# Performance work log

Hardware: AMD Instinct MI355X
Metric: run time of the kernel (lower is better)

Reference implementation:

```python
import jax, jax.numpy as jnp
import numpy as np

DIM = 1024

def setup_inputs() -> dict:
    key = jax.random.key(0)
    ks = jax.random.split(key, 8)
    B, Sx, Sy, D = 4, 2048, 2048, DIM
    s = 1.0 / np.sqrt(D)
    return {
        "x": jax.random.normal(ks[0], (B, Sx, D), jnp.float32),
        "y": jax.random.normal(ks[1], (B, Sy, D), jnp.float32),
        "Wq": jax.random.normal(ks[2], (D, D), jnp.float32) * s,
        "bq": jnp.zeros((D,), jnp.float32),
        "Wk": jax.random.normal(ks[3], (D, D), jnp.float32) * s,
        "bk": jnp.zeros((D,), jnp.float32),
        "Wv": jax.random.normal(ks[4], (D, D), jnp.float32) * s,
        "bv": jnp.zeros((D,), jnp.float32),
    }

def reference(x, y, Wq, bq, Wk, bk, Wv, bv):
    D = x.shape[-1]
    scale = jnp.sqrt(jnp.asarray(D, x.dtype))
    Q = jnp.einsum('bsd,de->bse', x, Wq) + bq  # [B,Sx,D]
    K = jnp.einsum('btd,de->bte', y, Wk) + bk  # [B,Sy,D]
    V = jnp.einsum('btd,de->bte', y, Wv) + bv  # [B,Sy,D]
    scores = jnp.einsum('bse,bte->bst', Q, K) / scale  # [B,Sx,Sy]
    probs = jax.nn.softmax(scores, axis=-1)
    out = jnp.einsum('bst,bte->bse', probs, V)  # [B,Sx,D]
    return out
```

## Files before the change

### kernel.cpp

```cpp
#include <hip/hip_runtime.h>

typedef __bf16 bf16x8_t __attribute__((ext_vector_type(8)));
typedef float f32x4_t __attribute__((ext_vector_type(4)));
typedef unsigned short ushort_t;

__device__ __forceinline__ unsigned short f2bf(float f) {
  unsigned u = __float_as_uint(f);
  u = (u + 0x7FFFu + ((u >> 16) & 1u)) >> 16;
  return (unsigned short)u;
}
__device__ __forceinline__ float bf2f(unsigned short h) {
  return __uint_as_float(((unsigned)h) << 16);
}

__device__ __forceinline__ void gload16(const void* g, void* l) {
  __builtin_amdgcn_global_load_lds(
      (const __attribute__((address_space(1))) unsigned int*)g,
      (__attribute__((address_space(3))) unsigned int*)l, 16, 0, 0);
}

#define BARRIER() __builtin_amdgcn_s_barrier()
#define LGKM0()                                        \
  do {                                                 \
    asm volatile("s_waitcnt lgkmcnt(0)" ::: "memory"); \
    __builtin_amdgcn_sched_barrier(0);                 \
  } while (0)

template<bool OUT_BF16, bool HAS_BIAS>
__global__ __launch_bounds__(512, 2)
void gemm256(const ushort_t* __restrict__ A, const ushort_t* __restrict__ Bt,
             void* __restrict__ Cp, const float* __restrict__ bias,
             int gx, int gy, int K, int lda, int ldb, int ldc,
             long sA, long sB, long sC, float alpha)
{
  __shared__ __align__(16) ushort_t sm[2 * 32768];
  const int tid = threadIdx.x;
  const int lane = tid & 63;
  const int w = tid >> 6;
  const int wr = w >> 2, wc = w & 3;

  const int per = gridDim.x >> 3;
  int wg = blockIdx.x;
  wg = (wg & 7) * per + (wg >> 3);
  const int bz = wg / (gx * gy);
  const int rr = wg - bz * gx * gy;
  const int by = rr / gx, bx = rr - by * gx;
  const int bm = by * 256, bn = bx * 256;

  const int srr = lane >> 3;
  const int csw = ((lane & 7) ^ srr) << 3;
  const ushort_t* pA = A + (long)bz * sA + (long)(bm + w * 16 + srr) * lda + csw;
  const ushort_t* pB = Bt + (long)bz * sB + (long)(bn + w * 16 + srr) * ldb + csw;

  auto stA = [&](int buf, int h, int t) {
    const ushort_t* g = pA + (long)(h * 128) * lda + t * 64;
    ushort_t* d = sm + buf * 32768 + h * 8192 + w * 1024;
    gload16(g, d);
    gload16(g + 8 * lda, d + 512);
  };
  auto stB = [&](int buf, int h, int t) {
    const ushort_t* g = pB + (long)(h * 128) * ldb + t * 64;
    ushort_t* d = sm + buf * 32768 + 16384 + h * 8192 + w * 1024;
    gload16(g, d);
    gload16(g + 8 * ldb, d + 512);
  };

  const int q = lane >> 4, x7 = lane & 7;
  const int cx0 = ((0 + q) ^ x7) << 3;
  const int cx1 = ((4 + q) ^ x7) << 3;
  const int abase = wr * 8192 + (lane & 15) * 64;
  const int bbase = 16384 + wc * 4096 + (lane & 15) * 64;

  f32x4_t acc[8][4];
  const f32x4_t z4 = {0.f, 0.f, 0.f, 0.f};
#pragma unroll
  for (int m = 0; m < 8; ++m)
#pragma unroll
    for (int n = 0; n < 4; ++n) acc[m][n] = z4;

  bf16x8_t a[8], blo[4], bhi[4];

  stA(0, 0, 0); stA(0, 1, 0); stB(0, 0, 0); stB(0, 1, 0);
  stB(1, 0, 1); stB(1, 1, 1); stA(1, 0, 1);
  asm volatile("s_waitcnt vmcnt(6)" ::: "memory");
  __builtin_amdgcn_sched_barrier(0);
  BARRIER();

#define LDX(off) __builtin_bit_cast(bf16x8_t, *(const uint4*)(s + (off)))

  const int nt = K >> 6;
  for (int t = 0; t < nt; ++t) {
    const int buf = t & 1;
    const ushort_t* s = sm + buf * 32768;

#pragma unroll
    for (int mf = 0; mf < 4; ++mf) {
      a[mf * 2]     = LDX(abase + mf * 1024 + cx0);
      a[mf * 2 + 1] = LDX(abase + mf * 1024 + cx1);
    }
#pragma unroll
    for (int nf = 0; nf < 2; ++nf) {
      blo[nf * 2]     = LDX(bbase + nf * 1024 + cx0);
      blo[nf * 2 + 1] = LDX(bbase + nf * 1024 + cx1);
    }
    if (t + 1 < nt) stA(buf ^ 1, 1, t + 1);
    BARRIER();
    LGKM0();
    __builtin_amdgcn_s_setprio(1);
#pragma unroll
    for (int mf = 0; mf < 4; ++mf)
#pragma unroll
      for (int nf = 0; nf < 2; ++nf) {
        acc[mf][nf] = __builtin_amdgcn_mfma_f32_16x16x32_bf16(a[mf * 2], blo[nf * 2], acc[mf][nf], 0, 0, 0);
        acc[mf][nf] = __builtin_amdgcn_mfma_f32_16x16x32_bf16(a[mf * 2 + 1], blo[nf * 2 + 1], acc[mf][nf], 0, 0, 0);
      }
    __builtin_amdgcn_s_setprio(0);
    BARRIER();

#pragma unroll
    for (int nf = 0; nf < 2; ++nf) {
      bhi[nf * 2]     = LDX(bbase + (nf + 2) * 1024 + cx0);
      bhi[nf * 2 + 1] = LDX(bbase + (nf + 2) * 1024 + cx1);
    }
    if (t + 2 < nt) stB(buf, 0, t + 2);
    BARRIER();
    LGKM0();
    __builtin_amdgcn_s_setprio(1);
#pragma unroll
    for (int mf = 0; mf < 4; ++mf)
#pragma unroll
      for (int nf = 0; nf < 2; ++nf) {
        acc[mf][nf + 2] = __builtin_amdgcn_mfma_f32_16x16x32_bf16(a[mf * 2], bhi[nf * 2], acc[mf][nf + 2], 0, 0, 0);
        acc[mf][nf + 2] = __builtin_amdgcn_mfma_f32_16x16x32_bf16(a[mf * 2 + 1], bhi[nf * 2 + 1], acc[mf][nf + 2], 0, 0, 0);
      }
    __builtin_amdgcn_s_setprio(0);
    BARRIER();

#pragma unroll
    for (int mf = 0; mf < 4; ++mf) {
      a[mf * 2]     = LDX(abase + (mf + 4) * 1024 + cx0);
      a[mf * 2 + 1] = LDX(abase + (mf + 4) * 1024 + cx1);
    }
    if (t + 2 < nt) stB(buf, 1, t + 2);
    BARRIER();
    LGKM0();
    __builtin_amdgcn_s_setprio(1);
#pragma unroll
    for (int mf = 0; mf < 4; ++mf)
#pragma unroll
      for (int nf = 0; nf < 2; ++nf) {
        acc[mf + 4][nf + 2] = __builtin_amdgcn_mfma_f32_16x16x32_bf16(a[mf * 2], bhi[nf * 2], acc[mf + 4][nf + 2], 0, 0, 0);
        acc[mf + 4][nf + 2] = __builtin_amdgcn_mfma_f32_16x16x32_bf16(a[mf * 2 + 1], bhi[nf * 2 + 1], acc[mf + 4][nf + 2], 0, 0, 0);
      }
    __builtin_amdgcn_s_setprio(0);
    BARRIER();

    if (t + 2 < nt) stA(buf, 0, t + 2);
    __builtin_amdgcn_s_setprio(1);
#pragma unroll
    for (int mf = 0; mf < 4; ++mf)
#pragma unroll
      for (int nf = 0; nf < 2; ++nf) {
        acc[mf + 4][nf] = __builtin_amdgcn_mfma_f32_16x16x32_bf16(a[mf * 2], blo[nf * 2], acc[mf + 4][nf], 0, 0, 0);
        acc[mf + 4][nf] = __builtin_amdgcn_mfma_f32_16x16x32_bf16(a[mf * 2 + 1], blo[nf * 2 + 1], acc[mf + 4][nf], 0, 0, 0);
      }
    __builtin_amdgcn_s_setprio(0);
    if (t + 1 < nt) {
      if (t + 2 < nt) asm volatile("s_waitcnt vmcnt(6)" ::: "memory");
      else            asm volatile("s_waitcnt vmcnt(0)" ::: "memory");
      __builtin_amdgcn_sched_barrier(0);
    }
    BARRIER();
  }
#undef LDX

  const long zC = (long)bz * sC;
  const int r0 = q * 4;
  const int c0 = lane & 15;
#pragma unroll
  for (int mf = 0; mf < 8; ++mf) {
    const int grow0 = bm + wr * 128 + mf * 16 + r0;
#pragma unroll
    for (int nf = 0; nf < 4; ++nf) {
      const int gcol = bn + wc * 64 + nf * 16 + c0;
      float bv_ = 0.f;
      if constexpr (HAS_BIAS) bv_ = bias[gcol];
#pragma unroll
      for (int i = 0; i < 4; ++i) {
        const float v = acc[mf][nf][i] * alpha + bv_;
        if constexpr (OUT_BF16) {
          ((ushort_t*)Cp)[zC + (long)(grow0 + i) * ldc + gcol] = f2bf(v);
        } else {
          ((float*)Cp)[zC + (long)(grow0 + i) * ldc + gcol] = v;
        }
      }
    }
  }
}

template<bool OUT_BF16, bool HAS_BIAS>
__global__ __launch_bounds__(512, 2)
void gemm_hs(const ushort_t* __restrict__ A, const ushort_t* __restrict__ Bt,
             void* __restrict__ Cp, const float* __restrict__ bias,
             int gx, int gy, int K, int lda, int ldb, int ldc,
             long sA, long sB, long sC, float alpha)
{
  __shared__ __align__(16) ushort_t sm[2 * 24576];
  const int tid = threadIdx.x;
  const int lane = tid & 63;
  const int w = tid >> 6;
  const int wr = w >> 2, wc = w & 3;

  const int per = gridDim.x >> 3;
  int wg = blockIdx.x;
  wg = (wg & 7) * per + (wg >> 3);
  const int bz = wg / (gx * gy);
  const int rr = wg - bz * gx * gy;
  const int by = rr / gx, bx = rr - by * gx;
  const int bm = by * 128, bn = bx * 256;

  const int srr = lane >> 3;
  const int csw = ((lane & 7) ^ srr) << 3;
  const ushort_t* pA = A + (long)bz * sA + (long)(bm + w * 16 + srr) * lda + csw;
  const ushort_t* pB = Bt + (long)bz * sB + (long)(bn + w * 32 + srr) * ldb + csw;

  auto stA = [&](int buf, int t) {
    const ushort_t* g = pA + t * 64;
    ushort_t* d = sm + buf * 24576 + w * 1024;
    gload16(g, d);
    gload16(g + 8 * lda, d + 512);
  };
  auto stB = [&](int buf, int t) {
    const ushort_t* g = pB + t * 64;
    ushort_t* d = sm + buf * 24576 + 8192 + w * 2048;
    gload16(g, d);
    gload16(g + 8 * ldb, d + 512);
    gload16(g + 16 * ldb, d + 1024);
    gload16(g + 24 * ldb, d + 1536);
  };

  const int q = lane >> 4, x7 = lane & 7;
  const int cx0 = ((0 + q) ^ x7) << 3;
  const int cx1 = ((4 + q) ^ x7) << 3;
  const int abase = wr * 4096 + (lane & 15) * 64;
  const int bbase = 8192 + wc * 4096 + (lane & 15) * 64;

  f32x4_t acc[4][4];
  const f32x4_t z4 = {0.f, 0.f, 0.f, 0.f};
#pragma unroll
  for (int m = 0; m < 4; ++m)
#pragma unroll
    for (int n = 0; n < 4; ++n) acc[m][n] = z4;

  bf16x8_t a01[4], a23[4], blo[4], bhi[4];

  stA(0, 0); stB(0, 0); stA(1, 1);
  asm volatile("s_waitcnt vmcnt(2)" ::: "memory");
  __builtin_amdgcn_sched_barrier(0);
  BARRIER();

#define LDX(off) __builtin_bit_cast(bf16x8_t, *(const uint4*)(s + (off)))

  const int nt = K >> 6;
  for (int t = 0; t < nt; ++t) {
    const int buf = t & 1;
    const ushort_t* s = sm + buf * 24576;

    a01[0] = LDX(abase + cx0);        a01[1] = LDX(abase + cx1);
    a01[2] = LDX(abase + 1024 + cx0); a01[3] = LDX(abase + 1024 + cx1);
    blo[0] = LDX(bbase + cx0);        blo[1] = LDX(bbase + cx1);
    blo[2] = LDX(bbase + 1024 + cx0); blo[3] = LDX(bbase + 1024 + cx1);
    if (t + 1 < nt) stB(buf ^ 1, t + 1);
    BARRIER();
    LGKM0();
    __builtin_amdgcn_s_setprio(1);
#pragma unroll
    for (int mf = 0; mf < 2; ++mf)
#pragma unroll
      for (int nf = 0; nf < 2; ++nf) {
        acc[mf][nf] = __builtin_amdgcn_mfma_f32_16x16x32_bf16(a01[mf * 2], blo[nf * 2], acc[mf][nf], 0, 0, 0);
        acc[mf][nf] = __builtin_amdgcn_mfma_f32_16x16x32_bf16(a01[mf * 2 + 1], blo[nf * 2 + 1], acc[mf][nf], 0, 0, 0);
      }
    __builtin_amdgcn_s_setprio(0);
    BARRIER();

    bhi[0] = LDX(bbase + 2048 + cx0); bhi[1] = LDX(bbase + 2048 + cx1);
    bhi[2] = LDX(bbase + 3072 + cx0); bhi[3] = LDX(bbase + 3072 + cx1);
    BARRIER();
    LGKM0();
    __builtin_amdgcn_s_setprio(1);
#pragma unroll
    for (int mf = 0; mf < 2; ++mf)
#pragma unroll
      for (int nf = 0; nf < 2; ++nf) {
        acc[mf][nf + 2] = __builtin_amdgcn_mfma_f32_16x16x32_bf16(a01[mf * 2], bhi[nf * 2], acc[mf][nf + 2], 0, 0, 0);
        acc[mf][nf + 2] = __builtin_amdgcn_mfma_f32_16x16x32_bf16(a01[mf * 2 + 1], bhi[nf * 2 + 1], acc[mf][nf + 2], 0, 0, 0);
      }
    __builtin_amdgcn_s_setprio(0);
    BARRIER();

    a23[0] = LDX(abase + 2048 + cx0); a23[1] = LDX(abase + 2048 + cx1);
    a23[2] = LDX(abase + 3072 + cx0); a23[3] = LDX(abase + 3072 + cx1);
    BARRIER();
    LGKM0();
    __builtin_amdgcn_s_setprio(1);
#pragma unroll
    for (int mf = 0; mf < 2; ++mf)
#pragma unroll
      for (int nf = 0; nf < 2; ++nf) {
        acc[mf + 2][nf + 2] = __builtin_amdgcn_mfma_f32_16x16x32_bf16(a23[mf * 2], bhi[nf * 2], acc[mf + 2][nf + 2], 0, 0, 0);
        acc[mf + 2][nf + 2] = __builtin_amdgcn_mfma_f32_16x16x32_bf16(a23[mf * 2 + 1], bhi[nf * 2 + 1], acc[mf + 2][nf + 2], 0, 0, 0);
      }
    __builtin_amdgcn_s_setprio(0);
    BARRIER();

    if (t + 2 < nt) stA(buf, t + 2);
    __builtin_amdgcn_s_setprio(1);
#pragma unroll
    for (int mf = 0; mf < 2; ++mf)
#pragma unroll
      for (int nf = 0; nf < 2; ++nf) {
        acc[mf + 2][nf] = __builtin_amdgcn_mfma_f32_16x16x32_bf16(a23[mf * 2], blo[nf * 2], acc[mf + 2][nf], 0, 0, 0);
        acc[mf + 2][nf] = __builtin_amdgcn_mfma_f32_16x16x32_bf16(a23[mf * 2 + 1], blo[nf * 2 + 1], acc[mf + 2][nf], 0, 0, 0);
      }
    __builtin_amdgcn_s_setprio(0);
    if (t + 1 < nt) {
      if (t + 2 < nt) asm volatile("s_waitcnt vmcnt(2)" ::: "memory");
      else            asm volatile("s_waitcnt vmcnt(0)" ::: "memory");
      __builtin_amdgcn_sched_barrier(0);
    }
    BARRIER();
  }
#undef LDX

  const long zC = (long)bz * sC;
  const int r0 = q * 4;
  const int c0 = lane & 15;
#pragma unroll
  for (int mf = 0; mf < 4; ++mf) {
    const int grow0 = bm + wr * 64 + mf * 16 + r0;
#pragma unroll
    for (int nf = 0; nf < 4; ++nf) {
      const int gcol = bn + wc * 64 + nf * 16 + c0;
      float bv_ = 0.f;
      if constexpr (HAS_BIAS) bv_ = bias[gcol];
#pragma unroll
      for (int i = 0; i < 4; ++i) {
        const float v = acc[mf][nf][i] * alpha + bv_;
        if constexpr (OUT_BF16) {
          ((ushort_t*)Cp)[zC + (long)(grow0 + i) * ldc + gcol] = f2bf(v);
        } else {
          ((float*)Cp)[zC + (long)(grow0 + i) * ldc + gcol] = v;
        }
      }
    }
  }
}

__global__ __launch_bounds__(256)
void conv2(const float* __restrict__ x, const float* __restrict__ y,
           ushort_t* __restrict__ xb, ushort_t* __restrict__ yb) {
  const int b = blockIdx.x;
  const float* in = (b < 4096) ? x : y;
  ushort_t* out = (b < 4096) ? xb : yb;
  const long i = (long)(b & 4095) * 256 + threadIdx.x;
  const float4 a = ((const float4*)in)[i * 2];
  const float4 c = ((const float4*)in)[i * 2 + 1];
  uint4 o;
  o.x = (unsigned)f2bf(a.x) | ((unsigned)f2bf(a.y) << 16);
  o.y = (unsigned)f2bf(a.z) | ((unsigned)f2bf(a.w) << 16);
  o.z = (unsigned)f2bf(c.x) | ((unsigned)f2bf(c.y) << 16);
  o.w = (unsigned)f2bf(c.z) | ((unsigned)f2bf(c.w) << 16);
  ((uint4*)out)[i] = o;
}

__global__ __launch_bounds__(256)
void wtrans3(const float* __restrict__ W0, const float* __restrict__ W1,
             const float* __restrict__ W2, ushort_t* __restrict__ T0,
             ushort_t* __restrict__ T1, ushort_t* __restrict__ T2) {
  const float* W = (blockIdx.z == 0) ? W0 : (blockIdx.z == 1) ? W1 : W2;
  ushort_t* Wt = (blockIdx.z == 0) ? T0 : (blockIdx.z == 1) ? T1 : T2;
  __shared__ float tile[32][33];
  const int bx = blockIdx.x * 32;
  const int by = blockIdx.y * 32;
  const int t = threadIdx.x;
  const int c = t & 31, r0 = t >> 5;
#pragma unroll
  for (int i = 0; i < 4; ++i)
    tile[r0 + i * 8][c] = W[(long)(by + r0 + i * 8) * 1024 + bx + c];
  __syncthreads();
#pragma unroll
  for (int i = 0; i < 4; ++i)
    Wt[(long)(bx + r0 + i * 8) * 1024 + by + c] = f2bf(tile[c][r0 + i * 8]);
}

__global__ __launch_bounds__(256)
void bconcat(const float* __restrict__ a, const float* __restrict__ b,
             float* __restrict__ o) {
  const int i = blockIdx.x * 256 + threadIdx.x;
  o[i] = (i < 1024) ? a[i] : b[i - 1024];
}

__global__ __launch_bounds__(256)
void transpose_bf16(const ushort_t* __restrict__ in, ushort_t* __restrict__ out,
                    int ld_in, int ld_out, long in_bs, long out_bs) {
  __shared__ ushort_t tt[64][65];
  in += (long)blockIdx.z * in_bs;
  out += (long)blockIdx.z * out_bs;
  const int r0 = blockIdx.y * 64, c0 = blockIdx.x * 64;
  const int tc = threadIdx.x & 31;
  const int tr = threadIdx.x >> 5;
#pragma unroll
  for (int i = 0; i < 8; ++i) {
    const unsigned v = *(const unsigned*)(in + (long)(r0 + tr + 8 * i) * ld_in + c0 + tc * 2);
    tt[tr + 8 * i][tc * 2] = (ushort_t)(v & 0xffff);
    tt[tr + 8 * i][tc * 2 + 1] = (ushort_t)(v >> 16);
  }
  __syncthreads();
#pragma unroll
  for (int i = 0; i < 8; ++i) {
    const unsigned v = (unsigned)tt[tc * 2][tr + 8 * i] |
                       ((unsigned)tt[tc * 2 + 1][tr + 8 * i] << 16);
    *(unsigned*)(out + (long)(c0 + tr + 8 * i) * ld_out + r0 + tc * 2) = v;
  }
}

__global__ __launch_bounds__(256)
void softmax_rows(ushort_t* __restrict__ S) {
  const long row = blockIdx.x;
  ushort_t* p = S + row * 2048;
  const int t = threadIdx.x;
  uint4 v = ((uint4*)p)[t];
  ushort_t* hp = (ushort_t*)&v;
  float f[8];
#pragma unroll
  for (int j = 0; j < 8; ++j) f[j] = bf2f(hp[j]);

  float m = f[0];
#pragma unroll
  for (int j = 1; j < 8; ++j) m = fmaxf(m, f[j]);
#pragma unroll
  for (int s = 32; s; s >>= 1) m = fmaxf(m, __shfl_xor(m, s, 64));
  __shared__ float redm[4];
  __shared__ float reds[4];
  const int wave = t >> 6, lane = t & 63;
  if (lane == 0) redm[wave] = m;
  __syncthreads();
  m = fmaxf(fmaxf(redm[0], redm[1]), fmaxf(redm[2], redm[3]));

  float sum = 0.f;
#pragma unroll
  for (int j = 0; j < 8; ++j) { f[j] = __expf(f[j] - m); sum += f[j]; }
#pragma unroll
  for (int s = 32; s; s >>= 1) sum += __shfl_xor(sum, s, 64);
  if (lane == 0) reds[wave] = sum;
  __syncthreads();
  sum = reds[0] + reds[1] + reds[2] + reds[3];
  const float inv = 1.0f / sum;
#pragma unroll
  for (int j = 0; j < 8; ++j) hp[j] = f2bf(f[j] * inv);
  ((uint4*)p)[t] = v;
}

extern "C" void kernel_launch(void* const* d_in, const int* in_sizes, int n_in,
                              void* d_out, int out_size, void* d_ws, size_t ws_size,
                              hipStream_t stream) {
  const float* x  = (const float*)d_in[0];
  const float* y  = (const float*)d_in[1];
  const float* Wq = (const float*)d_in[2];
  const float* bq = (const float*)d_in[3];
  const float* Wk = (const float*)d_in[4];
  const float* bk = (const float*)d_in[5];
  const float* Wv = (const float*)d_in[6];
  const float* bv = (const float*)d_in[7];
  float* out = (float*)d_out;

  const int D = 1024;
  const long MB_ = 1l << 20;

  ushort_t* ws  = (ushort_t*)d_ws;
  ushort_t* Wqt = ws;
  ushort_t* Wkv = ws + 1 * MB_;
  ushort_t* Wvt = ws + 2 * MB_;
  ushort_t* Qb  = ws + 3 * MB_;
  ushort_t* KV  = ws + 11 * MB_;
  ushort_t* yb  = ws + 27 * MB_;
  ushort_t* Vt  = ws + 27 * MB_;
  ushort_t* xb  = ws + 35 * MB_;
  ushort_t* Sb  = ws + 35 * MB_;
  float*    bkv = (float*)(ws + 51 * MB_);

  dim3 blk(256);

  conv2<<<dim3(8192), blk, 0, stream>>>(x, y, xb, yb);
  wtrans3<<<dim3(32, 32, 3), blk, 0, stream>>>(Wq, Wk, Wv, Wqt, Wkv, Wvt);
  bconcat<<<dim3(8), blk, 0, stream>>>(bk, bv, bkv);

  gemm_hs<true, true><<<dim3(256), dim3(512), 0, stream>>>(
      xb, Wqt, Qb, bq, 4, 64, D, D, D, D, 0, 0, 0, 1.0f);
  gemm256<true, true><<<dim3(256), dim3(512), 0, stream>>>(
      yb, Wkv, KV, bkv, 8, 32, D, D, D, 2048, 0, 0, 0, 1.0f);
  transpose_bf16<<<dim3(16, 32, 4), blk, 0, stream>>>(
      KV + 1024, Vt, 2048, 2048, 2048l * 2048, 1024l * 2048);

  gemm256<true, false><<<dim3(256), dim3(512), 0, stream>>>(
      Qb, KV, Sb, nullptr, 8, 8, D, D, 2048, 2048,
      2048l * 1024, 2048l * 2048, 2048l * 2048, 0.03125f);

  softmax_rows<<<dim3(8192), blk, 0, stream>>>(Sb);

  gemm_hs<false, false><<<dim3(256), dim3(512), 0, stream>>>(
      Sb, Vt, out, nullptr, 4, 16, 2048, 2048, 2048, D,
      2048l * 2048, 1024l * 2048, 2048l * 1024, 1.0f);
}
```

Before: 189.8 us.

## Restructure GEMM main loop to split K-halves across phases with new prefetch schedule

Reorganizes the inner loop of the bf16 MFMA GEMM so each of the four phases covers one K-half (cx0 or cx1) for one M-half across all four N fragments, instead of splitting by N-half. Register fragments become a0/a1/b0/b1. The global-to-LDS staging order changes too: both A halves of the next tile are now issued in the first two phases, and the vmcnt waits are adjusted to match. This is meant to rebalance LDS reads against MFMA work and change the overlap of loads. It risks different register pressure and more exposed load latency, since A tiles are now loaded only one iteration ahead.

```diff
diff --git a/kernel.cpp b/kernel.cpp
--- a/kernel.cpp
+++ b/kernel.cpp
@@ -65,9 +65,9 @@
     gload16(g + 8 * ldb, d + 512);
   };
 
-  const int q = lane >> 4, x7 = lane & 7;
-  const int cx0 = ((0 + q) ^ x7) << 3;
-  const int cx1 = ((4 + q) ^ x7) << 3;
+  const int q16 = lane >> 4, x7 = lane & 7;
+  const int cx0 = ((0 + q16) ^ x7) << 3;
+  const int cx1 = ((4 + q16) ^ x7) << 3;
   const int abase = wr * 8192 + (lane & 15) * 64;
   const int bbase = 16384 + wc * 4096 + (lane & 15) * 64;
 
@@ -78,11 +78,11 @@
 #pragma unroll
     for (int n = 0; n < 4; ++n) acc[m][n] = z4;
 
-  bf16x8_t a[8], blo[4], bhi[4];
+  bf16x8_t a0[4], a1[4], b0[4], b1[4];
 
   stA(0, 0, 0); stA(0, 1, 0); stB(0, 0, 0); stB(0, 1, 0);
-  stB(1, 0, 1); stB(1, 1, 1); stA(1, 0, 1);
-  asm volatile("s_waitcnt vmcnt(6)" ::: "memory");
+  stB(1, 0, 1); stB(1, 1, 1);
+  asm volatile("s_waitcnt vmcnt(4)" ::: "memory");
   __builtin_amdgcn_sched_barrier(0);
   BARRIER();
 
@@ -94,80 +94,68 @@
     const ushort_t* s = sm + buf * 32768;
 
 #pragma unroll
-    for (int mf = 0; mf < 4; ++mf) {
-      a[mf * 2]     = LDX(abase + mf * 1024 + cx0);
-      a[mf * 2 + 1] = LDX(abase + mf * 1024 + cx1);
-    }
-#pragma unroll
-    for (int nf = 0; nf < 2; ++nf) {
-      blo[nf * 2]     = LDX(bbase + nf * 1024 + cx0);
-      blo[nf * 2 + 1] = LDX(bbase + nf * 1024 + cx1);
-    }
+    for (int m = 0; m < 4; ++m) a0[m] = LDX(abase + m * 1024 + cx0);
+#pragma unroll
+    for (int n = 0; n < 4; ++n) b0[n] = LDX(bbase + n * 1024 + cx0);
+    if (t + 1 < nt) stA(buf ^ 1, 0, t + 1);
+    BARRIER();
+    LGKM0();
+    __builtin_amdgcn_s_setprio(1);
+#pragma unroll
+    for (int m = 0; m < 4; ++m)
+#pragma unroll
+      for (int n = 0; n < 4; ++n)
+        acc[m][n] = __builtin_amdgcn_mfma_f32_16x16x32_bf16(a0[m], b0[n], acc[m][n], 0, 0, 0);
+    __builtin_amdgcn_s_setprio(0);
+    BARRIER();
+
+#pragma unroll
+    for (int m = 0; m < 4; ++m) a1[m] = LDX(abase + m * 1024 + cx1);
+#pragma unroll
+    for (int n = 0; n < 4; ++n) b1[n] = LDX(bbase + n * 1024 + cx1);
     if (t + 1 < nt) stA(buf ^ 1, 1, t + 1);
     BARRIER();
     LGKM0();
     __builtin_amdgcn_s_setprio(1);
 #pragma unroll
-    for (int mf = 0; mf < 4; ++mf)
-#pragma unroll
-      for (int nf = 0; nf < 2; ++nf) {
-        acc[mf][nf] = __builtin_amdgcn_mfma_f32_16x16x32_bf16(a[mf * 2], blo[nf * 2], acc[mf][nf], 0, 0, 0);
-        acc[mf][nf] = __builtin_amdgcn_mfma_f32_16x16x32_bf16(a[mf * 2 + 1], blo[nf * 2 + 1], acc[mf][nf], 0, 0, 0);
-      }
-    __builtin_amdgcn_s_setprio(0);
-    BARRIER();
-
-#pragma unroll
-    for (int nf = 0; nf < 2; ++nf) {
-      bhi[nf * 2]     = LDX(bbase + (nf + 2) * 1024 + cx0);
-      bhi[nf * 2 + 1] = LDX(bbase + (nf + 2) * 1024 + cx1);
-    }
+    for (int m = 0; m < 4; ++m)
+#pragma unroll
+      for (int n = 0; n < 4; ++n)
+        acc[m][n] = __builtin_amdgcn_mfma_f32_16x16x32_bf16(a1[m], b1[n], acc[m][n], 0, 0, 0);
+    __builtin_amdgcn_s_setprio(0);
+    BARRIER();
+
+#pragma unroll
+    for (int m = 0; m < 4; ++m) a0[m] = LDX(abase + (m + 4) * 1024 + cx0);
     if (t + 2 < nt) stB(buf, 0, t + 2);
     BARRIER();
     LGKM0();
     __builtin_amdgcn_s_setprio(1);
 #pragma unroll
-    for (int mf = 0; mf < 4; ++mf)
-#pragma unroll
-      for (int nf = 0; nf < 2; ++nf) {
-        acc[mf][nf + 2] = __builtin_amdgcn_mfma_f32_16x16x32_bf16(a[mf * 2], bhi[nf * 2], acc[mf][nf + 2], 0, 0, 0);
-        acc[mf][nf + 2] = __builtin_amdgcn_mfma_f32_16x16x32_bf16(a[mf * 2 + 1], bhi[nf * 2 + 1], acc[mf][nf + 2], 0, 0, 0);
-      }
-    __builtin_amdgcn_s_setprio(0);
-    BARRIER();
-
-#pragma unroll
-    for (int mf = 0; mf < 4; ++mf) {
-      a[mf * 2]     = LDX(abase + (mf + 4) * 1024 + cx0);
-      a[mf * 2 + 1] = LDX(abase + (mf + 4) * 1024 + cx1);
-    }
+    for (int m = 0; m < 4; ++m)
+#pragma unroll
+      for (int n = 0; n < 4; ++n)
+        acc[m + 4][n] = __builtin_amdgcn_mfma_f32_16x16x32_bf16(a0[m], b0[n], acc[m + 4][n], 0, 0, 0);
+    __builtin_amdgcn_s_setprio(0);
+    BARRIER();
+
+#pragma unroll
+    for (int m = 0; m < 4; ++m) a1[m] = LDX(abase + (m + 4) * 1024 + cx1);
     if (t + 2 < nt) stB(buf, 1, t + 2);
     BARRIER();
     LGKM0();
     __builtin_amdgcn_s_setprio(1);
 #pragma unroll
-    for (int mf = 0; mf < 4; ++mf)
-#pragma unroll
-      for (int nf = 0; nf < 2; ++nf) {
-        acc[mf + 4][nf + 2] = __builtin_amdgcn_mfma_f32_16x16x32_bf16(a[mf * 2], bhi[nf * 2], acc[mf + 4][nf + 2], 0, 0, 0);
-        acc[mf + 4][nf + 2] = __builtin_amdgcn_mfma_f32_16x16x32_bf16(a[mf * 2 + 1], bhi[nf * 2 + 1], acc[mf + 4][nf + 2], 0, 0, 0);
-      }
-    __builtin_amdgcn_s_setprio(0);
-    BARRIER();
-
-    if (t + 2 < nt) stA(buf, 0, t + 2);
-    __builtin_amdgcn_s_setprio(1);
-#pragma unroll
-    for (int mf = 0; mf < 4; ++mf)
-#pragma unroll
-      for (int nf = 0; nf < 2; ++nf) {
-        acc[mf + 4][nf] = __builtin_amdgcn_mfma_f32_16x16x32_bf16(a[mf * 2], blo[nf * 2], acc[mf + 4][nf], 0, 0, 0);
-        acc[mf + 4][nf] = __builtin_amdgcn_mfma_f32_16x16x32_bf16(a[mf * 2 + 1], blo[nf * 2 + 1], acc[mf + 4][nf], 0, 0, 0);
-      }
-    __builtin_amdgcn_s_setprio(0);
-    if (t + 1 < nt) {
-      if (t + 2 < nt) asm volatile("s_waitcnt vmcnt(6)" ::: "memory");
-      else            asm volatile("s_waitcnt vmcnt(0)" ::: "memory");
+    for (int m = 0; m < 4; ++m)
+#pragma unroll
+      for (int n = 0; n < 4; ++n)
+        acc[m + 4][n] = __builtin_amdgcn_mfma_f32_16x16x32_bf16(a1[m], b1[n], acc[m + 4][n], 0, 0, 0);
+    __builtin_amdgcn_s_setprio(0);
+    if (t + 2 < nt) {
+      asm volatile("s_waitcnt vmcnt(4)" ::: "memory");
+      __builtin_amdgcn_sched_barrier(0);
+    } else if (t + 1 < nt) {
+      asm volatile("s_waitcnt vmcnt(0)" ::: "memory");
       __builtin_amdgcn_sched_barrier(0);
     }
     BARRIER();
@@ -175,7 +163,7 @@
 #undef LDX
 
   const long zC = (long)bz * sC;
-  const int r0 = q * 4;
+  const int r0 = q16 * 4;
   const int c0 = lane & 15;
 #pragma unroll
   for (int mf = 0; mf < 8; ++mf) {
```

Result: no change. 191.7 us (+1.0%).
